# Kernel tuning notes

Measured on AMD Instinct MI355X. Metric: run time of the kernel, lower is better.

Reference implementation:

```python
import jax, jax.numpy as jnp
import numpy as np

S = 2048          # total tokens (single sequence)
H = 2560          # hidden size
NH = 8            # query heads
NKV = 4           # kv heads
D = 256           # head dim
EPS = 1e-6
SCALING = 256.0 ** -0.5          # query_pre_attn_scalar ** -0.5
WINDOW = 1024 - 1                # config.sliding_window - 1
ROPE_THETA = 10000.0             # rope_local_base_freq (sliding layer)


def setup_inputs() -> dict:
    key = jax.random.key(0)
    ks = jax.random.split(key, 5)
    hidden_states = jax.random.normal(ks[0], (S, H), dtype=jnp.float32)
    # RoPE tables (default rope type, HF convention: freqs duplicated along last dim)
    inv_freq = 1.0 / (ROPE_THETA ** (np.arange(0, D, 2, dtype=np.float32) / D))
    pos = np.arange(S, dtype=np.float32)
    freqs = np.outer(pos, inv_freq)                 # [S, D/2]
    emb = np.concatenate([freqs, freqs], axis=-1)   # [S, D]
    cos = jnp.asarray(np.cos(emb), dtype=jnp.float32)
    sin = jnp.asarray(np.sin(emb), dtype=jnp.float32)
    w_qkv = jax.random.normal(ks[1], (H, (NH + 2 * NKV) * D), dtype=jnp.float32) * (H ** -0.5)
    w_o = jax.random.normal(ks[2], (NH * D, H), dtype=jnp.float32) * ((NH * D) ** -0.5)
    q_norm_w = jax.random.normal(ks[3], (D,), dtype=jnp.float32) * 0.02
    k_norm_w = jax.random.normal(ks[4], (D,), dtype=jnp.float32) * 0.02
    return {"hidden_states": hidden_states, "cos": cos, "sin": sin,
            "w_qkv": w_qkv, "w_o": w_o, "q_norm_w": q_norm_w, "k_norm_w": k_norm_w}


def _rms_norm(x, w):
    # Gemma3RMSNorm: x * rsqrt(mean(x^2)+eps) * (1 + w), computed in fp32
    var = jnp.mean(jnp.square(x), axis=-1, keepdims=True)
    return x * jax.lax.rsqrt(var + EPS) * (1.0 + w)


def _rotate_half(x):
    x1, x2 = jnp.split(x, 2, axis=-1)
    return jnp.concatenate([-x2, x1], axis=-1)


def reference(hidden_states, cos, sin, w_qkv, w_o, q_norm_w, k_norm_w):
    qkv = hidden_states @ w_qkv                          # [S, (NH+2NKV)*D]
    q, k, v = jnp.split(qkv, [NH * D, (NH + NKV) * D], axis=-1)
    q = q.reshape(S, NH, D)
    k = k.reshape(S, NKV, D)
    v = v.reshape(S, NKV, D)

    # per-head QK RMSNorm
    q = _rms_norm(q, q_norm_w)
    k = _rms_norm(k, k_norm_w)

    # RoPE (cos/sin broadcast over heads)
    c = cos[:, None, :]
    s = sin[:, None, :]
    q = q * c + _rotate_half(q) * s
    k = k * c + _rotate_half(k) * s

    # GQA expand kv heads
    rep = NH // NKV
    k = jnp.repeat(k, rep, axis=1)                       # [S, NH, D]
    v = jnp.repeat(v, rep, axis=1)

    scores = jnp.einsum('snd,tnd->nst', q, k) * SCALING  # [NH, S, S]
    i = jnp.arange(S)[:, None]
    j = jnp.arange(S)[None, :]
    allowed = (j <= i) & (i - j <= WINDOW)               # causal sliding window
    scores = jnp.where(allowed[None], scores, jnp.finfo(scores.dtype).min)
    probs = jax.nn.softmax(scores, axis=-1)
    attn = jnp.einsum('nst,tnd->snd', probs, v)          # [S, NH, D]
    out = attn.reshape(S, NH * D) @ w_o                  # [S, H]
    return out
```

## Files before the change

### kernel.cpp

```cpp
#include <hip/hip_runtime.h>
#include <hip/hip_bf16.h>
#include <cstdint>
#include <cstddef>

#define S_LEN 2048
#define HID   2560
#define NHQ   8
#define QKV_N 4096
#define ATT_N 2048
#define WIN   1023
#define SCALE 0.0625f
#define NINF  -3.0e38f

typedef __attribute__((ext_vector_type(8))) short bf16x8;
typedef __attribute__((ext_vector_type(4))) float f32x4;

__device__ __forceinline__ unsigned bf_hi(float f) {
  unsigned u = __builtin_bit_cast(unsigned, f);
  return (u + 0x7FFFu + ((u >> 16) & 1u)) >> 16;
}
__device__ __forceinline__ float bf_to_f(unsigned h) {
  return __builtin_bit_cast(float, h << 16);
}
__device__ __forceinline__ void g2l16(const void* g, void* l) {
  __builtin_amdgcn_global_load_lds((const __attribute__((address_space(1))) void*)g,
                                   (__attribute__((address_space(3))) void*)l,
                                   16, 0, 0);
}

__global__ __launch_bounds__(256) void split_rows(const float* __restrict__ X,
                                                  unsigned short* __restrict__ Xh,
                                                  unsigned short* __restrict__ Xl) {
  const size_t i = ((size_t)blockIdx.x * 256 + threadIdx.x) * 8;
  const float4 v0 = *(const float4*)(X + i);
  const float4 v1 = *(const float4*)(X + i + 4);
  const float f[8] = {v0.x, v0.y, v0.z, v0.w, v1.x, v1.y, v1.z, v1.w};
  unsigned hw[4], lw[4];
  #pragma unroll
  for (int j = 0; j < 4; ++j) {
    const unsigned h0 = bf_hi(f[2 * j]), h1 = bf_hi(f[2 * j + 1]);
    const float r0 = f[2 * j] - bf_to_f(h0), r1 = f[2 * j + 1] - bf_to_f(h1);
    hw[j] = h0 | (h1 << 16);
    lw[j] = bf_hi(r0) | (bf_hi(r1) << 16);
  }
  *(uint4*)(Xh + i) = make_uint4(hw[0], hw[1], hw[2], hw[3]);
  *(uint4*)(Xl + i) = make_uint4(lw[0], lw[1], lw[2], lw[3]);
}

__global__ __launch_bounds__(256) void split_transpose(const float* __restrict__ W,
                                                       unsigned short* __restrict__ Th,
                                                       unsigned short* __restrict__ Tl,
                                                       int K, int N) {
  __shared__ float tile[32][33];
  const int tid = threadIdx.x;
  const int kt = blockIdx.y * 32, nt = blockIdx.x * 32;
  {
    const int r = tid >> 3, c = (tid & 7) * 4;
    const float4 v = *(const float4*)(W + (size_t)(kt + r) * N + nt + c);
    tile[r][c] = v.x; tile[r][c + 1] = v.y; tile[r][c + 2] = v.z; tile[r][c + 3] = v.w;
  }
  __syncthreads();
  const int nl = tid >> 3, k = (tid & 7) * 4;
  unsigned hw[2], lw[2];
  #pragma unroll
  for (int j = 0; j < 2; ++j) {
    const float f0 = tile[k + 2 * j][nl], f1 = tile[k + 2 * j + 1][nl];
    const unsigned h0 = bf_hi(f0), h1 = bf_hi(f1);
    const float r0 = f0 - bf_to_f(h0), r1 = f1 - bf_to_f(h1);
    hw[j] = h0 | (h1 << 16);
    lw[j] = bf_hi(r0) | (bf_hi(r1) << 16);
  }
  *(uint2*)(Th + (size_t)(nt + nl) * K + kt + k) = make_uint2(hw[0], hw[1]);
  *(uint2*)(Tl + (size_t)(nt + nl) * K + kt + k) = make_uint2(lw[0], lw[1]);
}

__global__ __launch_bounds__(256) void gemm_bf16_split(
    const unsigned short* __restrict__ Ah, const unsigned short* __restrict__ Al,
    const unsigned short* __restrict__ Bh, const unsigned short* __restrict__ Bl,
    float* __restrict__ C, int M, int N, int K, int nbx) {
  __shared__ __align__(16) unsigned short smem[16384];

  const int tid = threadIdx.x;
  int bid = blockIdx.x;
  const int cpx = gridDim.x >> 3;
  bid = (bid & 7) * cpx + (bid >> 3);
  const int bm = (bid / nbx) * 128;
  const int bn = (bid % nbx) * 128;

  const int lane = tid & 63;
  const int wv = tid >> 6;
  const int wr = (wv >> 1) * 64;
  const int wc = (wv & 1) * 64;
  const int frow = lane & 15;
  const int g16 = lane >> 4;

  const int u0 = tid, u1 = tid + 256;
  const int r0 = u0 >> 2, s0 = (u0 & 3) ^ ((r0 >> 1) & 3);
  const int r1 = u1 >> 2, s1 = (u1 & 3) ^ ((r1 >> 1) & 3);

  const unsigned short* a_h = Ah + (size_t)bm * K;
  const unsigned short* a_l = Al + (size_t)bm * K;
  const unsigned short* b_h = Bh + (size_t)bn * K;
  const unsigned short* b_l = Bl + (size_t)bn * K;

  unsigned short* d0 = smem + ((tid & ~63) << 3);
  unsigned short* d1 = smem + 2048 + ((tid & ~63) << 3);

  const int sx = (g16 ^ ((frow >> 1) & 3)) * 8;

  f32x4 acc[4][4] = {};

  for (int k0 = 0; k0 < K; k0 += 32) {
    __syncthreads();
    {
      const size_t o0 = (size_t)r0 * K + k0 + s0 * 8;
      const size_t o1 = (size_t)r1 * K + k0 + s1 * 8;
      g2l16(a_h + o0, d0);
      g2l16(a_h + o1, d1);
      g2l16(a_l + o0, d0 + 4096);
      g2l16(a_l + o1, d1 + 4096);
      g2l16(b_h + o0, d0 + 8192);
      g2l16(b_h + o1, d1 + 8192);
      g2l16(b_l + o0, d0 + 12288);
      g2l16(b_l + o1, d1 + 12288);
    }
    __syncthreads();

    bf16x8 ah[4], al[4], bh[4], bl[4];
    #pragma unroll
    for (int i = 0; i < 4; ++i) {
      ah[i] = *(const bf16x8*)&smem[(wr + i * 16 + frow) * 32 + sx];
      al[i] = *(const bf16x8*)&smem[4096 + (wr + i * 16 + frow) * 32 + sx];
      bh[i] = *(const bf16x8*)&smem[8192 + (wc + i * 16 + frow) * 32 + sx];
      bl[i] = *(const bf16x8*)&smem[12288 + (wc + i * 16 + frow) * 32 + sx];
    }
    #pragma unroll
    for (int i = 0; i < 4; ++i)
      #pragma unroll
      for (int j = 0; j < 4; ++j) {
        acc[i][j] = __builtin_amdgcn_mfma_f32_16x16x32_bf16(ah[i], bh[j], acc[i][j], 0, 0, 0);
        acc[i][j] = __builtin_amdgcn_mfma_f32_16x16x32_bf16(ah[i], bl[j], acc[i][j], 0, 0, 0);
        acc[i][j] = __builtin_amdgcn_mfma_f32_16x16x32_bf16(al[i], bh[j], acc[i][j], 0, 0, 0);
      }
  }

  #pragma unroll
  for (int i = 0; i < 4; ++i) {
    const int row0 = bm + wr + i * 16 + g16 * 4;
    #pragma unroll
    for (int j = 0; j < 4; ++j) {
      const int c = bn + wc + j * 16 + frow;
      #pragma unroll
      for (int r = 0; r < 4; ++r)
        C[(size_t)(row0 + r) * N + c] = acc[i][j][r];
    }
  }
}

__global__ __launch_bounds__(256) void qk_norm_rope_split(
    const float* __restrict__ qkv, const float* __restrict__ cosp,
    const float* __restrict__ sinp, const float* __restrict__ qw,
    const float* __restrict__ kw,
    unsigned short* __restrict__ Qh, unsigned short* __restrict__ Ql,
    unsigned short* __restrict__ Kh, unsigned short* __restrict__ Kl) {
  const int lane = threadIdx.x & 63;
  const int wave = threadIdx.x >> 6;
  const int row  = blockIdx.x * 4 + wave;
  const int s    = row / 12;
  const int c    = row % 12;
  const float* p = qkv + (size_t)s * QKV_N + c * 256;

  float4 x = *(const float4*)(p + lane * 4);
  float ss = x.x * x.x + x.y * x.y + x.z * x.z + x.w * x.w;
  #pragma unroll
  for (int off = 32; off; off >>= 1) ss += __shfl_xor(ss, off);
  const float scale = rsqrtf(ss * (1.0f / 256.0f) + 1e-6f);

  const float* wp = (c < 8) ? qw : kw;
  float4 w4 = *(const float4*)(wp + lane * 4);
  float y0 = x.x * scale * (1.0f + w4.x);
  float y1 = x.y * scale * (1.0f + w4.y);
  float y2 = x.z * scale * (1.0f + w4.z);
  float y3 = x.w * scale * (1.0f + w4.w);

  float z0 = __shfl_xor(y0, 32);
  float z1 = __shfl_xor(y1, 32);
  float z2 = __shfl_xor(y2, 32);
  float z3 = __shfl_xor(y3, 32);
  const float sgn = (lane < 32) ? -1.0f : 1.0f;

  float4 c4 = *(const float4*)(cosp + (size_t)s * 256 + lane * 4);
  float4 s4 = *(const float4*)(sinp + (size_t)s * 256 + lane * 4);
  float o[4];
  o[0] = y0 * c4.x + sgn * z0 * s4.x;
  o[1] = y1 * c4.y + sgn * z1 * s4.y;
  o[2] = y2 * c4.z + sgn * z2 * s4.z;
  o[3] = y3 * c4.w + sgn * z3 * s4.w;

  const float mul = (c < 8) ? SCALE : 1.0f;
  #pragma unroll
  for (int j = 0; j < 4; ++j) o[j] *= mul;

  unsigned h[4], lo[4];
  #pragma unroll
  for (int j = 0; j < 4; ++j) {
    h[j] = bf_hi(o[j]);
    lo[j] = bf_hi(o[j] - bf_to_f(h[j]));
  }
  const size_t off = ((c < 8) ? ((size_t)c * S_LEN + s)
                              : ((size_t)(c - 8) * S_LEN + s)) * 256 + lane * 4;
  unsigned short* dh = (c < 8 ? Qh : Kh) + off;
  unsigned short* dl = (c < 8 ? Ql : Kl) + off;
  *(uint2*)dh = make_uint2(h[0] | (h[1] << 16), h[2] | (h[3] << 16));
  *(uint2*)dl = make_uint2(lo[0] | (lo[1] << 16), lo[2] | (lo[3] << 16));
}

__global__ __launch_bounds__(256) void v_split_transpose(
    const float* __restrict__ qkv,
    unsigned short* __restrict__ VTh, unsigned short* __restrict__ VTl) {
  __shared__ float tile[32][33];
  const int tid = threadIdx.x;
  const int s0 = blockIdx.x * 32, d0 = blockIdx.y * 32, kvh = blockIdx.z;
  {
    const int r = tid >> 3, c = (tid & 7) * 4;
    const float4 v = *(const float4*)(qkv + (size_t)(s0 + r) * QKV_N + 3072 + kvh * 256 + d0 + c);
    tile[r][c] = v.x; tile[r][c + 1] = v.y; tile[r][c + 2] = v.z; tile[r][c + 3] = v.w;
  }
  __syncthreads();
  const int dd = tid >> 3, sc = (tid & 7) * 4;
  unsigned h[4], lo[4];
  #pragma unroll
  for (int j = 0; j < 4; ++j) {
    const float f = tile[sc + j][dd];
    h[j] = bf_hi(f);
    lo[j] = bf_hi(f - bf_to_f(h[j]));
  }
  const size_t off = ((size_t)kvh * 256 + d0 + dd) * S_LEN + s0 + sc;
  *(uint2*)(VTh + off) = make_uint2(h[0] | (h[1] << 16), h[2] | (h[3] << 16));
  *(uint2*)(VTl + off) = make_uint2(lo[0] | (lo[1] << 16), lo[2] | (lo[3] << 16));
}

__global__ __launch_bounds__(64, 2) void attn_part(
    const unsigned short* __restrict__ Qh, const unsigned short* __restrict__ Ql,
    const unsigned short* __restrict__ Kh, const unsigned short* __restrict__ Kl,
    const unsigned short* __restrict__ VTh, const unsigned short* __restrict__ VTl,
    float* __restrict__ O0, float* __restrict__ O1, float* __restrict__ ML) {
  __shared__ __align__(16) unsigned short smem[1280];

  const int lane = threadIdx.x & 63;
  const int b    = blockIdx.x;
  const int xcd  = b & 7;
  const int kvh  = xcd >> 1;
  const int head = kvh * 2 + ((b >> 3) & 1);
  const int rest = b >> 4;
  const int kh   = rest & 1;
  const int qt   = ((rest >> 1) << 1) | (xcd & 1);
  const int q0   = qt * 16;
  const int g16  = lane >> 4;
  const int c16  = lane & 15;

  bf16x8 qh[8], ql[8];
  {
    const unsigned short* qph = Qh + ((size_t)head * S_LEN + q0 + c16) * 256 + g16 * 8;
    const unsigned short* qpl = Ql + ((size_t)head * S_LEN + q0 + c16) * 256 + g16 * 8;
    #pragma unroll
    for (int dc = 0; dc < 8; ++dc) {
      qh[dc] = *(const bf16x8*)(qph + dc * 32);
      ql[dc] = *(const bf16x8*)(qpl + dc * 32);
    }
  }

  f32x4 o_acc[16] = {};
  float m_run[4], l_run[4];
  #pragma unroll
  for (int r = 0; r < 4; ++r) { m_run[r] = NINF; l_run[r] = 0.0f; }

  const unsigned short* kh_g  = Kh  + (size_t)kvh * S_LEN * 256;
  const unsigned short* kl_g  = Kl  + (size_t)kvh * S_LEN * 256;
  const unsigned short* vth_g = VTh + (size_t)kvh * 256 * S_LEN;
  const unsigned short* vtl_g = VTl + (size_t)kvh * 256 * S_LEN;

  const int kstart = (q0 > WIN) ? ((q0 - WIN) & ~31) : 0;
  const int ntiles = ((q0 + 15 - kstart) >> 5) + 1;
  const int n0 = (ntiles + 1) >> 1;
  const int t_lo = kstart + (kh ? n0 * 32 : 0);
  const int t_hi = kstart + (kh ? ntiles * 32 : n0 * 32);

  for (int t0 = t_lo; t0 < t_hi; t0 += 32) {
    f32x4 sa[2] = {};
    #pragma unroll
    for (int t = 0; t < 2; ++t) {
      const unsigned short* kph = kh_g + (size_t)(t0 + t * 16 + c16) * 256 + g16 * 8;
      const unsigned short* kpl = kl_g + (size_t)(t0 + t * 16 + c16) * 256 + g16 * 8;
      #pragma unroll
      for (int dc = 0; dc < 8; ++dc) {
        const bf16x8 kfh = *(const bf16x8*)(kph + dc * 32);
        const bf16x8 kfl = *(const bf16x8*)(kpl + dc * 32);
        sa[t] = __builtin_amdgcn_mfma_f32_16x16x32_bf16(qh[dc], kfh, sa[t], 0, 0, 0);
        sa[t] = __builtin_amdgcn_mfma_f32_16x16x32_bf16(qh[dc], kfl, sa[t], 0, 0, 0);
        sa[t] = __builtin_amdgcn_mfma_f32_16x16x32_bf16(ql[dc], kfh, sa[t], 0, 0, 0);
      }
    }

    const int k0c = t0 + c16;
    #pragma unroll
    for (int r = 0; r < 4; ++r) {
      const int q = q0 + g16 * 4 + r;
      const bool v0 = (k0c <= q) && (q - k0c <= WIN);
      const bool v1 = (k0c + 16 <= q) && (q - (k0c + 16) <= WIN);
      float s0 = v0 ? sa[0][r] : NINF;
      float s1 = v1 ? sa[1][r] : NINF;
      float mx = fmaxf(s0, s1);
      #pragma unroll
      for (int off = 8; off; off >>= 1) mx = fmaxf(mx, __shfl_xor(mx, off));
      const float m_new = fmaxf(m_run[r], mx);
      const float rs = __expf(m_run[r] - m_new);
      const float p0 = v0 ? __expf(s0 - m_new) : 0.0f;
      const float p1 = v1 ? __expf(s1 - m_new) : 0.0f;
      float psum = p0 + p1;
      #pragma unroll
      for (int off = 8; off; off >>= 1) psum += __shfl_xor(psum, off);
      l_run[r] = l_run[r] * rs + psum;
      m_run[r] = m_new;
      #pragma unroll
      for (int dt = 0; dt < 16; ++dt) o_acc[dt][r] *= rs;
      const int pro = (g16 * 4 + r) * 40;
      const unsigned h0 = bf_hi(p0), h1 = bf_hi(p1);
      smem[pro + c16]       = (unsigned short)h0;
      smem[pro + 16 + c16]  = (unsigned short)h1;
      smem[640 + pro + c16]      = (unsigned short)bf_hi(p0 - bf_to_f(h0));
      smem[640 + pro + 16 + c16] = (unsigned short)bf_hi(p1 - bf_to_f(h1));
    }

    const bf16x8 pah = *(const bf16x8*)&smem[c16 * 40 + g16 * 8];
    const bf16x8 pal = *(const bf16x8*)&smem[640 + c16 * 40 + g16 * 8];
    #pragma unroll
    for (int dt = 0; dt < 16; ++dt) {
      const bf16x8 vfh = *(const bf16x8*)(vth_g + (size_t)(dt * 16 + c16) * S_LEN + t0 + g16 * 8);
      const bf16x8 vfl = *(const bf16x8*)(vtl_g + (size_t)(dt * 16 + c16) * S_LEN + t0 + g16 * 8);
      o_acc[dt] = __builtin_amdgcn_mfma_f32_16x16x32_bf16(pah, vfh, o_acc[dt], 0, 0, 0);
      o_acc[dt] = __builtin_amdgcn_mfma_f32_16x16x32_bf16(pah, vfl, o_acc[dt], 0, 0, 0);
      o_acc[dt] = __builtin_amdgcn_mfma_f32_16x16x32_bf16(pal, vfh, o_acc[dt], 0, 0, 0);
    }
  }

  float* op = (kh ? O1 : O0) + ((size_t)head * S_LEN + q0) * 256;
  #pragma unroll
  for (int r = 0; r < 4; ++r) {
    const int qloc = g16 * 4 + r;
    #pragma unroll
    for (int dt = 0; dt < 16; ++dt)
      op[(size_t)qloc * 256 + dt * 16 + c16] = o_acc[dt][r];
  }
  if (c16 == 0) {
    float* mlb = ML + kh * 32768;
    #pragma unroll
    for (int r = 0; r < 4; ++r) {
      const int q = q0 + g16 * 4 + r;
      mlb[head * S_LEN + q]         = m_run[r];
      mlb[16384 + head * S_LEN + q] = l_run[r];
    }
  }
}

__global__ __launch_bounds__(256) void attn_combine(
    const float* __restrict__ O0, const float* __restrict__ O1,
    const float* __restrict__ ML,
    unsigned short* __restrict__ Oh, unsigned short* __restrict__ Ol) {
  const int lane = threadIdx.x & 63;
  const int wave = threadIdx.x >> 6;
  const int row  = blockIdx.x * 4 + wave;
  const int head = row >> 11, s = row & 2047;
  const float m0 = ML[row],         l0 = ML[16384 + row];
  const float m1 = ML[32768 + row], l1 = ML[49152 + row];
  const float m  = fmaxf(m0, m1);
  const float w0 = __expf(m0 - m), w1 = __expf(m1 - m);
  const float inv = 1.0f / (l0 * w0 + l1 * w1);
  const float4 a = *(const float4*)(O0 + (size_t)row * 256 + lane * 4);
  const float4 bq = *(const float4*)(O1 + (size_t)row * 256 + lane * 4);
  float o[4] = {(a.x * w0 + bq.x * w1) * inv, (a.y * w0 + bq.y * w1) * inv,
                (a.z * w0 + bq.z * w1) * inv, (a.w * w0 + bq.w * w1) * inv};
  unsigned h[4], lo[4];
  #pragma unroll
  for (int j = 0; j < 4; ++j) {
    h[j] = bf_hi(o[j]);
    lo[j] = bf_hi(o[j] - bf_to_f(h[j]));
  }
  const size_t rowo = (size_t)s * ATT_N + head * 256 + lane * 4;
  *(uint2*)(Oh + rowo) = make_uint2(h[0] | (h[1] << 16), h[2] | (h[3] << 16));
  *(uint2*)(Ol + rowo) = make_uint2(lo[0] | (lo[1] << 16), lo[2] | (lo[3] << 16));
}

extern "C" void kernel_launch(void* const* d_in, const int* in_sizes, int n_in,
                              void* d_out, int out_size, void* d_ws, size_t ws_size,
                              hipStream_t stream) {
  const float* hs    = (const float*)d_in[0];
  const float* cosp  = (const float*)d_in[1];
  const float* sinp  = (const float*)d_in[2];
  const float* w_qkv = (const float*)d_in[3];
  const float* w_o   = (const float*)d_in[4];
  const float* qw    = (const float*)d_in[5];
  const float* kw    = (const float*)d_in[6];

  const size_t MB = 1024 * 1024;
  char* ws = (char*)d_ws;
  float* qkv = (float*)ws;
  unsigned short* wh = (unsigned short*)(ws + 32 * MB);
  unsigned short* wl = (unsigned short*)(ws + 52 * MB);
  unsigned short* Qh = (unsigned short*)(ws + 32 * MB);
  unsigned short* Ql = (unsigned short*)(ws + 40 * MB);
  unsigned short* Kh = (unsigned short*)(ws + 48 * MB);
  unsigned short* Kl = (unsigned short*)(ws + 52 * MB);
  unsigned short* VTh = (unsigned short*)(ws + 56 * MB);
  unsigned short* VTl = (unsigned short*)(ws + 60 * MB);
  float* O0 = (float*)ws;
  float* MLp = (float*)(ws + 16 * MB);
  unsigned short* Oh = (unsigned short*)(ws + 32 * MB);
  unsigned short* Ol = (unsigned short*)(ws + 40 * MB);
  unsigned short* oh = (unsigned short*)(ws + 48 * MB);
  unsigned short* ol = (unsigned short*)(ws + 58 * MB);
  unsigned short* Ahs = (unsigned short*)d_out;
  unsigned short* Als = Ahs + (size_t)S_LEN * HID;
  float* O1 = (float*)d_out;
  float* out = (float*)d_out;

  split_rows<<<(S_LEN * HID) / (256 * 8), 256, 0, stream>>>(hs, Ahs, Als);
  split_transpose<<<dim3(QKV_N / 32, HID / 32), 256, 0, stream>>>(
      w_qkv, wh, wl, HID, QKV_N);
  gemm_bf16_split<<<(S_LEN / 128) * (QKV_N / 128), 256, 0, stream>>>(
      Ahs, Als, wh, wl, qkv, S_LEN, QKV_N, HID, QKV_N / 128);
  qk_norm_rope_split<<<(S_LEN * 12) / 4, 256, 0, stream>>>(
      qkv, cosp, sinp, qw, kw, Qh, Ql, Kh, Kl);
  v_split_transpose<<<dim3(S_LEN / 32, 256 / 32, 4), 256, 0, stream>>>(
      qkv, VTh, VTl);
  attn_part<<<2048, 64, 0, stream>>>(Qh, Ql, Kh, Kl, VTh, VTl, O0, O1, MLp);
  attn_combine<<<(S_LEN * NHQ) / 4, 256, 0, stream>>>(O0, O1, MLp, Oh, Ol);
  split_transpose<<<dim3(HID / 32, ATT_N / 32), 256, 0, stream>>>(
      w_o, oh, ol, ATT_N, HID);
  gemm_bf16_split<<<(S_LEN / 128) * (HID / 128), 256, 0, stream>>>(
      Oh, Ol, oh, ol, out, S_LEN, HID, ATT_N, HID / 128);
}
```

Baseline: 574.6 us.

## Double-buffer GEMM LDS and share K tiles across two waves in attention

The split-bf16 GEMM now uses two LDS banks and prefetches the next K-slice while the current one is consumed, which drops one barrier per iteration and overlaps loads with MFMA. The attention partial kernel now uses 128-thread blocks covering 32 query rows. The K hi/lo tiles are staged into swizzled LDS once per block and read by both waves, instead of each wave loading K from global memory itself. This trades more LDS per block and extra barriers for less global traffic, and the larger query tile adds some masked work near the window edges.

```diff
diff --git a/kernel.cpp b/kernel.cpp
--- a/kernel.cpp
+++ b/kernel.cpp
@@ -78,7 +78,7 @@
     const unsigned short* __restrict__ Ah, const unsigned short* __restrict__ Al,
     const unsigned short* __restrict__ Bh, const unsigned short* __restrict__ Bl,
     float* __restrict__ C, int M, int N, int K, int nbx) {
-  __shared__ __align__(16) unsigned short smem[16384];
+  __shared__ __align__(16) unsigned short smem[32768];
 
   const int tid = threadIdx.x;
   int bid = blockIdx.x;
@@ -103,36 +103,38 @@
   const unsigned short* b_h = Bh + (size_t)bn * K;
   const unsigned short* b_l = Bl + (size_t)bn * K;
 
-  unsigned short* d0 = smem + ((tid & ~63) << 3);
-  unsigned short* d1 = smem + 2048 + ((tid & ~63) << 3);
-
+  const int db0 = (tid & ~63) << 3;
   const int sx = (g16 ^ ((frow >> 1) & 3)) * 8;
 
   f32x4 acc[4][4] = {};
 
+#define STAGE(bank, kk)                                                     \
+  {                                                                         \
+    unsigned short* sb = smem + (bank) * 16384;                             \
+    unsigned short* dd0 = sb + db0;                                         \
+    unsigned short* dd1 = sb + 2048 + db0;                                  \
+    const size_t o0 = (size_t)r0 * K + (kk) + s0 * 8;                       \
+    const size_t o1 = (size_t)r1 * K + (kk) + s1 * 8;                       \
+    g2l16(a_h + o0, dd0);          g2l16(a_h + o1, dd1);                    \
+    g2l16(a_l + o0, dd0 + 4096);   g2l16(a_l + o1, dd1 + 4096);             \
+    g2l16(b_h + o0, dd0 + 8192);   g2l16(b_h + o1, dd1 + 8192);             \
+    g2l16(b_l + o0, dd0 + 12288);  g2l16(b_l + o1, dd1 + 12288);            \
+  }
+
+  STAGE(0, 0);
+  int cur = 0;
   for (int k0 = 0; k0 < K; k0 += 32) {
     __syncthreads();
-    {
-      const size_t o0 = (size_t)r0 * K + k0 + s0 * 8;
-      const size_t o1 = (size_t)r1 * K + k0 + s1 * 8;
-      g2l16(a_h + o0, d0);
-      g2l16(a_h + o1, d1);
-      g2l16(a_l + o0, d0 + 4096);
-      g2l16(a_l + o1, d1 + 4096);
-      g2l16(b_h + o0, d0 + 8192);
-      g2l16(b_h + o1, d1 + 8192);
-      g2l16(b_l + o0, d0 + 12288);
-      g2l16(b_l + o1, d1 + 12288);
-    }
-    __syncthreads();
-
+    if (k0 + 32 < K) STAGE(cur ^ 1, k0 + 32);
+
+    const unsigned short* sb = smem + cur * 16384;
     bf16x8 ah[4], al[4], bh[4], bl[4];
     #pragma unroll
     for (int i = 0; i < 4; ++i) {
-      ah[i] = *(const bf16x8*)&smem[(wr + i * 16 + frow) * 32 + sx];
-      al[i] = *(const bf16x8*)&smem[4096 + (wr + i * 16 + frow) * 32 + sx];
-      bh[i] = *(const bf16x8*)&smem[8192 + (wc + i * 16 + frow) * 32 + sx];
-      bl[i] = *(const bf16x8*)&smem[12288 + (wc + i * 16 + frow) * 32 + sx];
+      ah[i] = *(const bf16x8*)&sb[(wr + i * 16 + frow) * 32 + sx];
+      al[i] = *(const bf16x8*)&sb[4096 + (wr + i * 16 + frow) * 32 + sx];
+      bh[i] = *(const bf16x8*)&sb[8192 + (wc + i * 16 + frow) * 32 + sx];
+      bl[i] = *(const bf16x8*)&sb[12288 + (wc + i * 16 + frow) * 32 + sx];
     }
     #pragma unroll
     for (int i = 0; i < 4; ++i)
@@ -142,7 +144,9 @@
         acc[i][j] = __builtin_amdgcn_mfma_f32_16x16x32_bf16(ah[i], bl[j], acc[i][j], 0, 0, 0);
         acc[i][j] = __builtin_amdgcn_mfma_f32_16x16x32_bf16(al[i], bh[j], acc[i][j], 0, 0, 0);
       }
-  }
+    cur ^= 1;
+  }
+#undef STAGE
 
   #pragma unroll
   for (int i = 0; i < 4; ++i) {
@@ -240,29 +244,31 @@
   *(uint2*)(VTl + off) = make_uint2(lo[0] | (lo[1] << 16), lo[2] | (lo[3] << 16));
 }
 
-__global__ __launch_bounds__(64, 2) void attn_part(
+__global__ __launch_bounds__(128, 2) void attn_part(
     const unsigned short* __restrict__ Qh, const unsigned short* __restrict__ Ql,
     const unsigned short* __restrict__ Kh, const unsigned short* __restrict__ Kl,
     const unsigned short* __restrict__ VTh, const unsigned short* __restrict__ VTl,
     float* __restrict__ O0, float* __restrict__ O1, float* __restrict__ ML) {
-  __shared__ __align__(16) unsigned short smem[1280];
-
-  const int lane = threadIdx.x & 63;
+  __shared__ __align__(16) unsigned short smem[18944];
+
+  const int tid  = threadIdx.x;
+  const int lane = tid & 63;
+  const int wv   = __builtin_amdgcn_readfirstlane(tid >> 6);
   const int b    = blockIdx.x;
   const int xcd  = b & 7;
   const int kvh  = xcd >> 1;
   const int head = kvh * 2 + ((b >> 3) & 1);
-  const int rest = b >> 4;
-  const int kh   = rest & 1;
-  const int qt   = ((rest >> 1) << 1) | (xcd & 1);
-  const int q0   = qt * 16;
+  const int kh   = (b >> 4) & 1;
+  const int qt   = (((b >> 5) << 1) | (xcd & 1));
+  const int q0   = qt * 32;
   const int g16  = lane >> 4;
   const int c16  = lane & 15;
+  const int rmin = q0 + wv * 16;
 
   bf16x8 qh[8], ql[8];
   {
-    const unsigned short* qph = Qh + ((size_t)head * S_LEN + q0 + c16) * 256 + g16 * 8;
-    const unsigned short* qpl = Ql + ((size_t)head * S_LEN + q0 + c16) * 256 + g16 * 8;
+    const unsigned short* qph = Qh + ((size_t)head * S_LEN + rmin + c16) * 256 + g16 * 8;
+    const unsigned short* qpl = Ql + ((size_t)head * S_LEN + rmin + c16) * 256 + g16 * 8;
     #pragma unroll
     for (int dc = 0; dc < 8; ++dc) {
       qh[dc] = *(const bf16x8*)(qph + dc * 32);
@@ -281,21 +287,42 @@
   const unsigned short* vtl_g = VTl + (size_t)kvh * 256 * S_LEN;
 
   const int kstart = (q0 > WIN) ? ((q0 - WIN) & ~31) : 0;
-  const int ntiles = ((q0 + 15 - kstart) >> 5) + 1;
+  const int ntiles = ((q0 + 31 - kstart) >> 5) + 1;
   const int n0 = (ntiles + 1) >> 1;
   const int t_lo = kstart + (kh ? n0 * 32 : 0);
   const int t_hi = kstart + (kh ? ntiles * 32 : n0 * 32);
 
+  const int PB = 16384 + wv * 1280;
+
   for (int t0 = t_lo; t0 < t_hi; t0 += 32) {
+    __syncthreads();
+    {
+      char* lbase = (char*)smem + ((tid & ~63) << 4);
+      #pragma unroll
+      for (int i = 0; i < 8; ++i) {
+        const int uu = i * 128 + tid, row = uu >> 5, sl = uu & 31;
+        g2l16(kh_g + (size_t)(t0 + row) * 256 + ((sl ^ (row & 7)) * 8),
+              lbase + i * 2048);
+      }
+      #pragma unroll
+      for (int i = 0; i < 8; ++i) {
+        const int uu = i * 128 + tid, row = uu >> 5, sl = uu & 31;
+        g2l16(kl_g + (size_t)(t0 + row) * 256 + ((sl ^ (row & 7)) * 8),
+              lbase + 16384 + i * 2048);
+      }
+    }
+    __syncthreads();
+
     f32x4 sa[2] = {};
     #pragma unroll
     for (int t = 0; t < 2; ++t) {
-      const unsigned short* kph = kh_g + (size_t)(t0 + t * 16 + c16) * 256 + g16 * 8;
-      const unsigned short* kpl = kl_g + (size_t)(t0 + t * 16 + c16) * 256 + g16 * 8;
+      const int krow = t * 16 + c16;
+      const int swz = krow & 7;
       #pragma unroll
       for (int dc = 0; dc < 8; ++dc) {
-        const bf16x8 kfh = *(const bf16x8*)(kph + dc * 32);
-        const bf16x8 kfl = *(const bf16x8*)(kpl + dc * 32);
+        const int sl = ((dc * 4 + g16) ^ swz) * 16;
+        const bf16x8 kfh = *(const bf16x8*)((const char*)smem + krow * 512 + sl);
+        const bf16x8 kfl = *(const bf16x8*)((const char*)smem + 16384 + krow * 512 + sl);
         sa[t] = __builtin_amdgcn_mfma_f32_16x16x32_bf16(qh[dc], kfh, sa[t], 0, 0, 0);
         sa[t] = __builtin_amdgcn_mfma_f32_16x16x32_bf16(qh[dc], kfl, sa[t], 0, 0, 0);
         sa[t] = __builtin_amdgcn_mfma_f32_16x16x32_bf16(ql[dc], kfh, sa[t], 0, 0, 0);
@@ -305,7 +332,7 @@
     const int k0c = t0 + c16;
     #pragma unroll
     for (int r = 0; r < 4; ++r) {
-      const int q = q0 + g16 * 4 + r;
+      const int q = rmin + g16 * 4 + r;
       const bool v0 = (k0c <= q) && (q - k0c <= WIN);
       const bool v1 = (k0c + 16 <= q) && (q - (k0c + 16) <= WIN);
       float s0 = v0 ? sa[0][r] : NINF;
@@ -324,7 +351,7 @@
       m_run[r] = m_new;
       #pragma unroll
       for (int dt = 0; dt < 16; ++dt) o_acc[dt][r] *= rs;
-      const int pro = (g16 * 4 + r) * 40;
+      const int pro = PB + (g16 * 4 + r) * 40;
       const unsigned h0 = bf_hi(p0), h1 = bf_hi(p1);
       smem[pro + c16]       = (unsigned short)h0;
       smem[pro + 16 + c16]  = (unsigned short)h1;
@@ -332,8 +359,8 @@
       smem[640 + pro + 16 + c16] = (unsigned short)bf_hi(p1 - bf_to_f(h1));
     }
 
-    const bf16x8 pah = *(const bf16x8*)&smem[c16 * 40 + g16 * 8];
-    const bf16x8 pal = *(const bf16x8*)&smem[640 + c16 * 40 + g16 * 8];
+    const bf16x8 pah = *(const bf16x8*)&smem[PB + c16 * 40 + g16 * 8];
+    const bf16x8 pal = *(const bf16x8*)&smem[PB + 640 + c16 * 40 + g16 * 8];
     #pragma unroll
     for (int dt = 0; dt < 16; ++dt) {
       const bf16x8 vfh = *(const bf16x8*)(vth_g + (size_t)(dt * 16 + c16) * S_LEN + t0 + g16 * 8);
@@ -344,7 +371,7 @@
     }
   }
 
-  float* op = (kh ? O1 : O0) + ((size_t)head * S_LEN + q0) * 256;
+  float* op = (kh ? O1 : O0) + ((size_t)head * S_LEN + rmin) * 256;
   #pragma unroll
   for (int r = 0; r < 4; ++r) {
     const int qloc = g16 * 4 + r;
@@ -356,7 +383,7 @@
     float* mlb = ML + kh * 32768;
     #pragma unroll
     for (int r = 0; r < 4; ++r) {
-      const int q = q0 + g16 * 4 + r;
+      const int q = rmin + g16 * 4 + r;
       mlb[head * S_LEN + q]         = m_run[r];
       mlb[16384 + head * S_LEN + q] = l_run[r];
     }
@@ -433,7 +460,7 @@
       qkv, cosp, sinp, qw, kw, Qh, Ql, Kh, Kl);
   v_split_transpose<<<dim3(S_LEN / 32, 256 / 32, 4), 256, 0, stream>>>(
       qkv, VTh, VTl);
-  attn_part<<<2048, 64, 0, stream>>>(Qh, Ql, Kh, Kl, VTh, VTl, O0, O1, MLp);
+  attn_part<<<1024, 128, 0, stream>>>(Qh, Ql, Kh, Kl, VTh, VTl, O0, O1, MLp);
   attn_combine<<<(S_LEN * NHQ) / 4, 256, 0, stream>>>(O0, O1, MLp, Oh, Ol);
   split_transpose<<<dim3(HID / 32, ATT_N / 32), 256, 0, stream>>>(
       w_o, oh, ol, ATT_N, HID);
```

Result: faster. 535.8 us (-6.7%).
